# Kernel optimization log

Hardware: AMD Instinct MI355X
Metric: run time of the kernel (lower is better)

Reference implementation:

```python
import jax, jax.numpy as jnp
import numpy as np
import math

B, T, D, H = 4, 2048, 1024, 16
HD = D // H  # head_dim = 64

def setup_inputs() -> dict:
    key = jax.random.key(0)
    k1, k2, k3, k4, k5 = jax.random.split(key, 5)
    s = 1.0 / math.sqrt(D)
    return {
        "x": jax.random.normal(k1, (B, T, D), dtype=jnp.float32),
        "W_qkv": jax.random.normal(k2, (D, 3 * D), dtype=jnp.float32) * s,
        "b_qkv": jax.random.normal(k3, (3 * D,), dtype=jnp.float32) * 0.01,
        "W_fc": jax.random.normal(k4, (D, D), dtype=jnp.float32) * s,
        "b_fc": jax.random.normal(k5, (D,), dtype=jnp.float32) * 0.01,
    }

def reference(x, W_qkv, b_qkv, W_fc, b_fc):
    Bx, Tx, C = x.shape
    qkv = x @ W_qkv + b_qkv                                   # [B,T,3D]
    qkv = qkv.reshape(Bx, Tx, 3, H, HD)
    q, k, v = qkv[:, :, 0], qkv[:, :, 1], qkv[:, :, 2]        # [B,T,H,hd]
    scale = 1.0 / math.sqrt(HD)
    scores = jnp.einsum('bqhd,bkhd->bhqk', q, k) * scale      # [B,H,T,T]
    causal = jnp.tril(jnp.ones((Tx, Tx), dtype=bool))
    scores = jnp.where(causal, scores, -jnp.inf)
    weights = jax.nn.softmax(scores, axis=-1)
    out = jnp.einsum('bhqk,bkhd->bqhd', weights, v).reshape(Bx, Tx, C)
    return out @ W_fc + b_fc
```

## Files before the change

kernel.cpp:

```cpp
#include <hip/hip_runtime.h>
#include <hip/hip_bf16.h>

typedef __hip_bfloat16 bf16;
typedef short bf16x8 __attribute__((ext_vector_type(8)));
typedef float f32x4 __attribute__((ext_vector_type(4)));


static __device__ __forceinline__ void glds16(const bf16* g, bf16* l) {
  __builtin_amdgcn_global_load_lds(
      (const __attribute__((address_space(1))) void*)g,
      (__attribute__((address_space(3))) void*)l, 16, 0, 0);
}

static __device__ __forceinline__ unsigned short f2b(float f) {
  return __builtin_bit_cast(unsigned short, __float2bfloat16(f));
}
static __device__ __forceinline__ float b2f(unsigned int u16bits) {
  return __builtin_bit_cast(float, u16bits << 16);
}
static __device__ __forceinline__ float ex2(float x) {
  return __builtin_amdgcn_exp2f(x);
}

__global__ void k_convert(const float* __restrict__ in, unsigned short* __restrict__ out, int n4) {
  int i = blockIdx.x * 256 + threadIdx.x;
  if (i >= n4) return;
  float4 v = reinterpret_cast<const float4*>(in)[i];
  ushort4 o;
  o.x = f2b(v.x); o.y = f2b(v.y); o.z = f2b(v.z); o.w = f2b(v.w);
  reinterpret_cast<ushort4*>(out)[i] = o;
}

__global__ void k_transpose(const float* __restrict__ in, bf16* __restrict__ out, int R, int C) {
  __shared__ float t[32][33];
  int c0 = blockIdx.x * 32, r0 = blockIdx.y * 32;
  int tx = threadIdx.x, ty = threadIdx.y;
  #pragma unroll
  for (int j = 0; j < 32; j += 8)
    t[ty + j][tx] = in[(size_t)(r0 + ty + j) * C + c0 + tx];
  __syncthreads();
  #pragma unroll
  for (int j = 0; j < 32; j += 8)
    out[(size_t)(c0 + ty + j) * R + r0 + tx] = __float2bfloat16(t[tx][ty + j]);
}

template<int EPI>
__global__ __launch_bounds__(256, 2)
void k_gemm(const bf16* __restrict__ A, const bf16* __restrict__ Bt,
            const float* __restrict__ bias,
            bf16* __restrict__ Qh, bf16* __restrict__ Kh, bf16* __restrict__ Vt,
            float* __restrict__ Out)
{
  constexpr int K = 1024;
  __shared__ bf16 sA[128 * 32];
  __shared__ bf16 sB[128 * 32];
  const int tid = threadIdx.x;
  const int wv = tid >> 6, lane = tid & 63;
  const int wr = wv >> 1, wc = wv & 1;
  const int l4 = lane >> 4, l15 = lane & 15;

  const int nbx = gridDim.x;
  const int nwg = nbx * gridDim.y;
  const int flat = blockIdx.y * nbx + blockIdx.x;
  const int cpx = nwg >> 3;
  const int swz = (flat & 7) * cpx + (flat >> 3);
  const int bx = swz % nbx;
  const int by = swz / nbx;

  const int srow = lane >> 2;
  const int scol = (lane & 3) * 8;
  const bf16* gA0 = A  + (size_t)(by * 128 + wv * 16 + srow) * K + scol;
  const bf16* gB0 = Bt + (size_t)(bx * 128 + wv * 16 + srow) * K + scol;
  bf16* lA0 = sA + wv * 16 * 32;
  bf16* lB0 = sB + wv * 16 * 32;

  f32x4 acc[4][4];
  #pragma unroll
  for (int i = 0; i < 4; ++i)
    #pragma unroll
    for (int j = 0; j < 4; ++j) acc[i][j] = f32x4{0.f, 0.f, 0.f, 0.f};

  for (int kb = 0; kb < K; kb += 32) {
    glds16(gA0 + kb,                   lA0);
    glds16(gA0 + kb + (size_t)64 * K,  lA0 + 64 * 32);
    glds16(gB0 + kb,                   lB0);
    glds16(gB0 + kb + (size_t)64 * K,  lB0 + 64 * 32);
    __syncthreads();
    bf16x8 af[4], bfr[4];
    #pragma unroll
    for (int i = 0; i < 4; ++i)
      af[i] = *reinterpret_cast<const bf16x8*>(sA + (wr * 64 + i * 16 + l15) * 32 + l4 * 8);
    #pragma unroll
    for (int j = 0; j < 4; ++j)
      bfr[j] = *reinterpret_cast<const bf16x8*>(sB + (wc * 64 + j * 16 + l15) * 32 + l4 * 8);
    #pragma unroll
    for (int i = 0; i < 4; ++i)
      #pragma unroll
      for (int j = 0; j < 4; ++j)
        acc[i][j] = __builtin_amdgcn_mfma_f32_16x16x32_bf16(af[i], bfr[j], acc[i][j], 0, 0, 0);
    __syncthreads();
  }

  if (EPI == 0) {
    #pragma unroll
    for (int j = 0; j < 4; ++j) {
      const int n = bx * 128 + wc * 64 + j * 16 + l15;
      const float bj = bias[n];
      const int s = n >> 10;
      const int hh = (n >> 6) & 15;
      const int d = n & 63;
      #pragma unroll
      for (int i = 0; i < 4; ++i) {
        #pragma unroll
        for (int r = 0; r < 4; ++r) {
          const int m = by * 128 + wr * 64 + i * 16 + l4 * 4 + r;
          const int bb = m >> 11, t = m & 2047;
          const bf16 o = __float2bfloat16(acc[i][j][r] + bj);
          if (s == 0)      Qh[((size_t)((bb * 16 + hh) * 2048 + t)) * 64 + d] = o;
          else if (s == 1) Kh[((size_t)((bb * 16 + hh) * 2048 + t)) * 64 + d] = o;
          else             Vt[((size_t)((bb * 16 + hh) * 64 + d)) * 2048 + t] = o;
        }
      }
    }
  } else {
    #pragma unroll
    for (int j = 0; j < 4; ++j) {
      const int n = bx * 128 + wc * 64 + j * 16 + l15;
      const float bj = bias[n];
      #pragma unroll
      for (int i = 0; i < 4; ++i)
        #pragma unroll
        for (int r = 0; r < 4; ++r) {
          const int m = by * 128 + wr * 64 + i * 16 + l4 * 4 + r;
          Out[(size_t)m * 1024 + n] = acc[i][j][r] + bj;
        }
    }
  }
}

__global__ __launch_bounds__(256, 3)
void k_attn(const bf16* __restrict__ Qh, const bf16* __restrict__ Kh,
            const bf16* __restrict__ Vt, bf16* __restrict__ Ao)
{
  __shared__ unsigned int smem[4608];
  const int tid = threadIdx.x;
  const int wv = tid >> 6, lane = tid & 63;
  const int l4 = lane >> 4, l15 = lane & 15;

  const int bid = blockIdx.x;
  const int xcd = bid & 7;
  const int idx = bid >> 3;
  const int g   = idx & 31;
  const int grp = idx >> 5;
  const int bh  = grp * 8 + xcd;
  const int b = bh >> 4, h = bh & 15;

  const int role = (wv + bid) & 3;
  const int qi = (role < 2) ? g : (63 - g);
  const int parity = role & 1;
  const int qbase = qi * 32;

  const bf16* Qp = Qh + (size_t)bh * 2048 * 64;
  const bf16* Kp = Kh + (size_t)bh * 2048 * 64;
  const bf16* Vp = Vt + (size_t)bh * 64 * 2048;
  bf16* Pw = (bf16*)smem + wv * (32 * 40);

  bf16x8 qa[2][2];
  #pragma unroll
  for (int i = 0; i < 2; ++i)
    #pragma unroll
    for (int kh = 0; kh < 2; ++kh)
      qa[i][kh] = *reinterpret_cast<const bf16x8*>(
          Qp + (size_t)(qbase + i * 16 + l15) * 64 + kh * 32 + l4 * 8);

  f32x4 o[2][4];
  float mr[2], lr[2];
  #pragma unroll
  for (int i = 0; i < 2; ++i) {
    #pragma unroll
    for (int jd = 0; jd < 4; ++jd) o[i][jd] = f32x4{0.f, 0.f, 0.f, 0.f};
    mr[i] = -1e30f; lr[i] = 0.f;
  }

  const int ktmax = (qbase + 31) >> 5;

  const int kt0 = (parity <= ktmax) ? parity : ktmax;
  bf16x8 kbf[2][2];
  #pragma unroll
  for (int j = 0; j < 2; ++j)
    #pragma unroll
    for (int kh = 0; kh < 2; ++kh)
      kbf[j][kh] = *reinterpret_cast<const bf16x8*>(
          Kp + (size_t)(kt0 * 32 + j * 16 + l15) * 64 + kh * 32 + l4 * 8);

  for (int kt = parity; kt <= ktmax; kt += 2) {
    const bool full = (kt * 32 + 31) <= qbase;

    f32x4 s[2][2];
    #pragma unroll
    for (int i = 0; i < 2; ++i)
      #pragma unroll
      for (int j = 0; j < 2; ++j) s[i][j] = f32x4{0.f, 0.f, 0.f, 0.f};
    #pragma unroll
    for (int j = 0; j < 2; ++j)
      #pragma unroll
      for (int i = 0; i < 2; ++i) {
        s[i][j] = __builtin_amdgcn_mfma_f32_16x16x32_bf16(kbf[j][0], qa[i][0], s[i][j], 0, 0, 0);
        s[i][j] = __builtin_amdgcn_mfma_f32_16x16x32_bf16(kbf[j][1], qa[i][1], s[i][j], 0, 0, 0);
      }

    bf16x8 vbf[4];
    #pragma unroll
    for (int jd = 0; jd < 4; ++jd)
      vbf[jd] = *reinterpret_cast<const bf16x8*>(
          Vp + (size_t)(jd * 16 + l15) * 2048 + kt * 32 + l4 * 8);

    #pragma unroll
    for (int i = 0; i < 2; ++i) {
      const int q = qbase + i * 16 + l15;
      #pragma unroll
      for (int j = 0; j < 2; ++j)
        #pragma unroll
        for (int r = 0; r < 4; ++r) {
          float v = s[i][j][r] * 0.18033688f;
          if (!full) {
            const int kk = kt * 32 + j * 16 + l4 * 4 + r;
            if (kk > q) v = -1e30f;
          }
          s[i][j][r] = v;
        }
    }

    #pragma unroll
    for (int i = 0; i < 2; ++i) {
      float mx = s[i][0][0];
      #pragma unroll
      for (int j = 0; j < 2; ++j)
        #pragma unroll
        for (int r = 0; r < 4; ++r)
          if (j + r > 0) mx = fmaxf(mx, s[i][j][r]);
      mx = fmaxf(mx, __shfl_xor(mx, 16));
      mx = fmaxf(mx, __shfl_xor(mx, 32));
      if (__any(mx > mr[i] + 8.f)) {
        const float mn = fmaxf(mr[i], mx);
        const float al = ex2(mr[i] - mn);
        mr[i] = mn;
        lr[i] *= al;
        float albc[4];
        #pragma unroll
        for (int r = 0; r < 4; ++r) albc[r] = __shfl(al, l4 * 4 + r);
        #pragma unroll
        for (int jd = 0; jd < 4; ++jd)
          #pragma unroll
          for (int r = 0; r < 4; ++r) o[i][jd][r] *= albc[r];
      }
      float ps = 0.f;
      #pragma unroll
      for (int j = 0; j < 2; ++j) {
        const float p0 = ex2(s[i][j][0] - mr[i]);
        const float p1 = ex2(s[i][j][1] - mr[i]);
        const float p2 = ex2(s[i][j][2] - mr[i]);
        const float p3 = ex2(s[i][j][3] - mr[i]);
        ps += (p0 + p1) + (p2 + p3);
        const unsigned int u0 = (unsigned int)f2b(p0) | ((unsigned int)f2b(p1) << 16);
        const unsigned int u1 = (unsigned int)f2b(p2) | ((unsigned int)f2b(p3) << 16);
        *reinterpret_cast<uint2*>(Pw + (i * 16 + l15) * 40 + j * 16 + l4 * 4) =
            make_uint2(u0, u1);
      }
      ps += __shfl_xor(ps, 16);
      ps += __shfl_xor(ps, 32);
      lr[i] += ps;
    }

    const int ktn = (kt + 2 <= ktmax) ? (kt + 2) : ktmax;
    #pragma unroll
    for (int j = 0; j < 2; ++j)
      #pragma unroll
      for (int kh = 0; kh < 2; ++kh)
        kbf[j][kh] = *reinterpret_cast<const bf16x8*>(
            Kp + (size_t)(ktn * 32 + j * 16 + l15) * 64 + kh * 32 + l4 * 8);

    bf16x8 pa[2];
    #pragma unroll
    for (int i = 0; i < 2; ++i)
      pa[i] = *reinterpret_cast<const bf16x8*>(Pw + (i * 16 + l15) * 40 + l4 * 8);
    #pragma unroll
    for (int jd = 0; jd < 4; ++jd)
      #pragma unroll
      for (int i = 0; i < 2; ++i)
        o[i][jd] = __builtin_amdgcn_mfma_f32_16x16x32_bf16(pa[i], vbf[jd], o[i][jd], 0, 0, 0);
  }

  float mrv[2][4], lrv[2][4];
  #pragma unroll
  for (int i = 0; i < 2; ++i)
    #pragma unroll
    for (int r = 0; r < 4; ++r) {
      mrv[i][r] = __shfl(mr[i], l4 * 4 + r);
      lrv[i][r] = __shfl(lr[i], l4 * 4 + r);
    }

  __syncthreads();
  unsigned int* reg0 = smem;
  unsigned int* reg1 = smem + 64 * 33;
  if (parity == 1) {
    unsigned int* p = ((role == 1) ? reg0 : reg1) + lane * 33;
    #pragma unroll
    for (int i = 0; i < 2; ++i)
      #pragma unroll
      for (int r = 0; r < 4; ++r) {
        p[i * 4 + r]     = __builtin_bit_cast(unsigned int, mrv[i][r]);
        p[8 + i * 4 + r] = __builtin_bit_cast(unsigned int, lrv[i][r]);
      }
    #pragma unroll
    for (int i = 0; i < 2; ++i)
      #pragma unroll
      for (int jd = 0; jd < 4; ++jd)
        #pragma unroll
        for (int rp = 0; rp < 2; ++rp) {
          unsigned int lo = f2b(o[i][jd][2 * rp]);
          unsigned int hi = f2b(o[i][jd][2 * rp + 1]);
          p[16 + (i * 4 + jd) * 2 + rp] = lo | (hi << 16);
        }
  }
  __syncthreads();
  if (parity == 0) {
    const unsigned int* p = ((role == 0) ? reg0 : reg1) + lane * 33;
    #pragma unroll
    for (int i = 0; i < 2; ++i)
      #pragma unroll
      for (int r = 0; r < 4; ++r) {
        const float m1 = __builtin_bit_cast(float, p[i * 4 + r]);
        const float l1 = __builtin_bit_cast(float, p[8 + i * 4 + r]);
        const float mm = fmaxf(mrv[i][r], m1);
        const float a0 = ex2(mrv[i][r] - mm);
        const float a1 = ex2(m1 - mm);
        const float inv = 1.f / (lrv[i][r] * a0 + l1 * a1);
        const int q = qbase + i * 16 + l4 * 4 + r;
        #pragma unroll
        for (int jd = 0; jd < 4; ++jd) {
          const unsigned int u = p[16 + (i * 4 + jd) * 2 + (r >> 1)];
          const float o1 = b2f((r & 1) ? (u >> 16) : (u & 0xffffu));
          const float val = (o[i][jd][r] * a0 + o1 * a1) * inv;
          Ao[(size_t)(b * 2048 + q) * 1024 + h * 64 + jd * 16 + l15] = __float2bfloat16(val);
        }
      }
  }
}

extern "C" void kernel_launch(void* const* d_in, const int* in_sizes, int n_in,
                              void* d_out, int out_size, void* d_ws, size_t ws_size,
                              hipStream_t stream)
{
  const float* x     = (const float*)d_in[0];
  const float* W_qkv = (const float*)d_in[1];
  const float* b_qkv = (const float*)d_in[2];
  const float* W_fc  = (const float*)d_in[3];
  const float* b_fc  = (const float*)d_in[4];
  float* out = (float*)d_out;

  char* ws = (char*)d_ws;
  bf16* x_bf = (bf16*)ws;  ws += (size_t)8192 * 1024 * 2;
  bf16* Wqt  = (bf16*)ws;  ws += (size_t)3072 * 1024 * 2;
  bf16* Wft  = (bf16*)ws;  ws += (size_t)1024 * 1024 * 2;
  bf16* Qh   = (bf16*)ws;  ws += (size_t)4 * 16 * 2048 * 64 * 2;
  bf16* Kh   = (bf16*)ws;  ws += (size_t)4 * 16 * 2048 * 64 * 2;
  bf16* Vt   = (bf16*)ws;  ws += (size_t)4 * 16 * 64 * 2048 * 2;
  bf16* Ao   = (bf16*)ws;  ws += (size_t)8192 * 1024 * 2;

  k_convert<<<8192, 256, 0, stream>>>(x, (unsigned short*)x_bf, 8192 * 1024 / 4);
  k_transpose<<<dim3(3072 / 32, 1024 / 32), dim3(32, 8), 0, stream>>>(W_qkv, Wqt, 1024, 3072);
  k_transpose<<<dim3(1024 / 32, 1024 / 32), dim3(32, 8), 0, stream>>>(W_fc, Wft, 1024, 1024);
  k_gemm<0><<<dim3(24, 64), 256, 0, stream>>>(x_bf, Wqt, b_qkv, Qh, Kh, Vt, nullptr);
  k_attn<<<2048, 256, 0, stream>>>(Qh, Kh, Vt, Ao);
  k_gemm<1><<<dim3(8, 64), 256, 0, stream>>>(Ao, Wft, b_fc, nullptr, nullptr, nullptr, out);
}
```

Before: 272.9 us.

## Split causal attention KV range across four waves per query tile

Each attention block now processes a single 32-row query tile, with its four waves striding over key tiles by four instead of pairing two query tiles with two waves each. Partial softmax states from three waves are merged through shared memory by the fourth, and the grid doubles. This aims for finer scheduling granularity and shorter per-wave loops, at the cost of idle waves on short causal rows, a heavier merge step and larger LDS use.

```diff
diff --git a/kernel.cpp b/kernel.cpp
--- a/kernel.cpp
+++ b/kernel.cpp
@@ -142,7 +142,7 @@
 void k_attn(const bf16* __restrict__ Qh, const bf16* __restrict__ Kh,
             const bf16* __restrict__ Vt, bf16* __restrict__ Ao)
 {
-  __shared__ unsigned int smem[4608];
+  __shared__ unsigned int smem[6336];
   const int tid = threadIdx.x;
   const int wv = tid >> 6, lane = tid & 63;
   const int l4 = lane >> 4, l15 = lane & 15;
@@ -150,14 +150,12 @@
   const int bid = blockIdx.x;
   const int xcd = bid & 7;
   const int idx = bid >> 3;
-  const int g   = idx & 31;
-  const int grp = idx >> 5;
+  const int qi  = idx & 63;
+  const int grp = idx >> 6;
   const int bh  = grp * 8 + xcd;
   const int b = bh >> 4, h = bh & 15;
 
   const int role = (wv + bid) & 3;
-  const int qi = (role < 2) ? g : (63 - g);
-  const int parity = role & 1;
   const int qbase = qi * 32;
 
   const bf16* Qp = Qh + (size_t)bh * 2048 * 64;
@@ -182,9 +180,9 @@
     mr[i] = -1e30f; lr[i] = 0.f;
   }
 
-  const int ktmax = (qbase + 31) >> 5;
-
-  const int kt0 = (parity <= ktmax) ? parity : ktmax;
+  const int ktmax = qi;
+
+  const int kt0 = (role <= ktmax) ? role : ktmax;
   bf16x8 kbf[2][2];
   #pragma unroll
   for (int j = 0; j < 2; ++j)
@@ -193,7 +191,7 @@
       kbf[j][kh] = *reinterpret_cast<const bf16x8*>(
           Kp + (size_t)(kt0 * 32 + j * 16 + l15) * 64 + kh * 32 + l4 * 8);
 
-  for (int kt = parity; kt <= ktmax; kt += 2) {
+  for (int kt = role; kt <= ktmax; kt += 4) {
     const bool full = (kt * 32 + 31) <= qbase;
 
     f32x4 s[2][2];
@@ -272,7 +270,7 @@
       lr[i] += ps;
     }
 
-    const int ktn = (kt + 2 <= ktmax) ? (kt + 2) : ktmax;
+    const int ktn = (kt + 4 <= ktmax) ? (kt + 4) : ktmax;
     #pragma unroll
     for (int j = 0; j < 2; ++j)
       #pragma unroll
@@ -301,10 +299,8 @@
     }
 
   __syncthreads();
-  unsigned int* reg0 = smem;
-  unsigned int* reg1 = smem + 64 * 33;
-  if (parity == 1) {
-    unsigned int* p = ((role == 1) ? reg0 : reg1) + lane * 33;
+  if (role != 0) {
+    unsigned int* p = smem + (role - 1) * (64 * 33) + lane * 33;
     #pragma unroll
     for (int i = 0; i < 2; ++i)
       #pragma unroll
@@ -324,24 +320,35 @@
         }
   }
   __syncthreads();
-  if (parity == 0) {
-    const unsigned int* p = ((role == 0) ? reg0 : reg1) + lane * 33;
+  if (role == 0) {
+    const unsigned int* p0 = smem + 0 * (64 * 33) + lane * 33;
+    const unsigned int* p1 = smem + 1 * (64 * 33) + lane * 33;
+    const unsigned int* p2 = smem + 2 * (64 * 33) + lane * 33;
     #pragma unroll
     for (int i = 0; i < 2; ++i)
       #pragma unroll
       for (int r = 0; r < 4; ++r) {
-        const float m1 = __builtin_bit_cast(float, p[i * 4 + r]);
-        const float l1 = __builtin_bit_cast(float, p[8 + i * 4 + r]);
-        const float mm = fmaxf(mrv[i][r], m1);
+        const float m1 = __builtin_bit_cast(float, p0[i * 4 + r]);
+        const float m2 = __builtin_bit_cast(float, p1[i * 4 + r]);
+        const float m3 = __builtin_bit_cast(float, p2[i * 4 + r]);
+        const float l1 = __builtin_bit_cast(float, p0[8 + i * 4 + r]);
+        const float l2 = __builtin_bit_cast(float, p1[8 + i * 4 + r]);
+        const float l3 = __builtin_bit_cast(float, p2[8 + i * 4 + r]);
+        const float mm = fmaxf(fmaxf(mrv[i][r], m1), fmaxf(m2, m3));
         const float a0 = ex2(mrv[i][r] - mm);
         const float a1 = ex2(m1 - mm);
-        const float inv = 1.f / (lrv[i][r] * a0 + l1 * a1);
+        const float a2 = ex2(m2 - mm);
+        const float a3 = ex2(m3 - mm);
+        const float inv = 1.f / (lrv[i][r] * a0 + l1 * a1 + l2 * a2 + l3 * a3);
         const int q = qbase + i * 16 + l4 * 4 + r;
         #pragma unroll
         for (int jd = 0; jd < 4; ++jd) {
-          const unsigned int u = p[16 + (i * 4 + jd) * 2 + (r >> 1)];
-          const float o1 = b2f((r & 1) ? (u >> 16) : (u & 0xffffu));
-          const float val = (o[i][jd][r] * a0 + o1 * a1) * inv;
+          const int ui = 16 + (i * 4 + jd) * 2 + (r >> 1);
+          const bool hi = (r & 1);
+          const float o1 = b2f(hi ? (p0[ui] >> 16) : (p0[ui] & 0xffffu));
+          const float o2 = b2f(hi ? (p1[ui] >> 16) : (p1[ui] & 0xffffu));
+          const float o3 = b2f(hi ? (p2[ui] >> 16) : (p2[ui] & 0xffffu));
+          const float val = (o[i][jd][r] * a0 + o1 * a1 + o2 * a2 + o3 * a3) * inv;
           Ao[(size_t)(b * 2048 + q) * 1024 + h * 64 + jd * 16 + l15] = __float2bfloat16(val);
         }
       }
@@ -372,6 +379,6 @@
   k_transpose<<<dim3(3072 / 32, 1024 / 32), dim3(32, 8), 0, stream>>>(W_qkv, Wqt, 1024, 3072);
   k_transpose<<<dim3(1024 / 32, 1024 / 32), dim3(32, 8), 0, stream>>>(W_fc, Wft, 1024, 1024);
   k_gemm<0><<<dim3(24, 64), 256, 0, stream>>>(x_bf, Wqt, b_qkv, Qh, Kh, Vt, nullptr);
-  k_attn<<<2048, 256, 0, stream>>>(Qh, Kh, Vt, Ao);
+  k_attn<<<4096, 256, 0, stream>>>(Qh, Kh, Vt, Ao);
   k_gemm<1><<<dim3(8, 64), 256, 0, stream>>>(Ao, Wft, b_fc, nullptr, nullptr, nullptr, out);
 }
```

After: 289.8 us. +6.2%, slower.

## Double GEMM K-tile to 64 with XOR-swizzled LDS and fold softmax scale into Q

Applied to the files above, without the earlier changes.

The GEMM kernel now stages a K depth of 64 per iteration instead of 32, which halves the number of barrier pairs per output tile. The shared-memory layout gets an XOR swizzle on the 16-byte granules so fragment reads avoid bank conflicts. The softmax scale factor (1/sqrt(d) times log2 e) is folded into Q in the QKV epilogue, removing one multiply per score element in the attention inner loop. In exchange, LDS use per block doubles, and rounding Q to bf16 after scaling slightly changes numerics.

```diff
diff --git a/kernel.cpp b/kernel.cpp
--- a/kernel.cpp
+++ b/kernel.cpp
@@ -52,8 +52,8 @@
             float* __restrict__ Out)
 {
   constexpr int K = 1024;
-  __shared__ bf16 sA[128 * 32];
-  __shared__ bf16 sB[128 * 32];
+  __shared__ bf16 sA[128 * 64];
+  __shared__ bf16 sB[128 * 64];
   const int tid = threadIdx.x;
   const int wv = tid >> 6, lane = tid & 63;
   const int wr = wv >> 1, wc = wv & 1;
@@ -67,12 +67,12 @@
   const int bx = swz % nbx;
   const int by = swz / nbx;
 
-  const int srow = lane >> 2;
-  const int scol = (lane & 3) * 8;
-  const bf16* gA0 = A  + (size_t)(by * 128 + wv * 16 + srow) * K + scol;
-  const bf16* gB0 = Bt + (size_t)(bx * 128 + wv * 16 + srow) * K + scol;
-  bf16* lA0 = sA + wv * 16 * 32;
-  bf16* lB0 = sB + wv * 16 * 32;
+  const int srow8 = lane >> 3;
+  const int sgran = (lane & 7) ^ srow8;
+  const bf16* gA0 = A  + (size_t)(by * 128 + wv * 8 + srow8) * K + sgran * 8;
+  const bf16* gB0 = Bt + (size_t)(bx * 128 + wv * 8 + srow8) * K + sgran * 8;
+  bf16* lA0 = sA + wv * 8 * 64;
+  bf16* lB0 = sB + wv * 8 * 64;
 
   f32x4 acc[4][4];
   #pragma unroll
@@ -80,24 +80,34 @@
     #pragma unroll
     for (int j = 0; j < 4; ++j) acc[i][j] = f32x4{0.f, 0.f, 0.f, 0.f};
 
-  for (int kb = 0; kb < K; kb += 32) {
-    glds16(gA0 + kb,                   lA0);
-    glds16(gA0 + kb + (size_t)64 * K,  lA0 + 64 * 32);
-    glds16(gB0 + kb,                   lB0);
-    glds16(gB0 + kb + (size_t)64 * K,  lB0 + 64 * 32);
+  for (int kb = 0; kb < K; kb += 64) {
+    #pragma unroll
+    for (int c = 0; c < 4; ++c) {
+      glds16(gA0 + kb + (size_t)(c * 32) * K, lA0 + c * 32 * 64);
+      glds16(gB0 + kb + (size_t)(c * 32) * K, lB0 + c * 32 * 64);
+    }
     __syncthreads();
-    bf16x8 af[4], bfr[4];
-    #pragma unroll
-    for (int i = 0; i < 4; ++i)
-      af[i] = *reinterpret_cast<const bf16x8*>(sA + (wr * 64 + i * 16 + l15) * 32 + l4 * 8);
-    #pragma unroll
-    for (int j = 0; j < 4; ++j)
-      bfr[j] = *reinterpret_cast<const bf16x8*>(sB + (wc * 64 + j * 16 + l15) * 32 + l4 * 8);
-    #pragma unroll
-    for (int i = 0; i < 4; ++i)
-      #pragma unroll
-      for (int j = 0; j < 4; ++j)
-        acc[i][j] = __builtin_amdgcn_mfma_f32_16x16x32_bf16(af[i], bfr[j], acc[i][j], 0, 0, 0);
+    #pragma unroll
+    for (int kk = 0; kk < 2; ++kk) {
+      bf16x8 af[4], bfr[4];
+      #pragma unroll
+      for (int i = 0; i < 4; ++i) {
+        const int R = wr * 64 + i * 16 + l15;
+        af[i] = *reinterpret_cast<const bf16x8*>(
+            sA + R * 64 + (((kk * 4 + l4) ^ (R & 7)) * 8));
+      }
+      #pragma unroll
+      for (int j = 0; j < 4; ++j) {
+        const int R = wc * 64 + j * 16 + l15;
+        bfr[j] = *reinterpret_cast<const bf16x8*>(
+            sB + R * 64 + (((kk * 4 + l4) ^ (R & 7)) * 8));
+      }
+      #pragma unroll
+      for (int i = 0; i < 4; ++i)
+        #pragma unroll
+        for (int j = 0; j < 4; ++j)
+          acc[i][j] = __builtin_amdgcn_mfma_f32_16x16x32_bf16(af[i], bfr[j], acc[i][j], 0, 0, 0);
+    }
     __syncthreads();
   }
 
@@ -115,7 +125,9 @@
         for (int r = 0; r < 4; ++r) {
           const int m = by * 128 + wr * 64 + i * 16 + l4 * 4 + r;
           const int bb = m >> 11, t = m & 2047;
-          const bf16 o = __float2bfloat16(acc[i][j][r] + bj);
+          float of = acc[i][j][r] + bj;
+          if (s == 0) of *= 0.18033688f;
+          const bf16 o = __float2bfloat16(of);
           if (s == 0)      Qh[((size_t)((bb * 16 + hh) * 2048 + t)) * 64 + d] = o;
           else if (s == 1) Kh[((size_t)((bb * 16 + hh) * 2048 + t)) * 64 + d] = o;
           else             Vt[((size_t)((bb * 16 + hh) * 64 + d)) * 2048 + t] = o;
@@ -222,7 +234,7 @@
       for (int j = 0; j < 2; ++j)
         #pragma unroll
         for (int r = 0; r < 4; ++r) {
-          float v = s[i][j][r] * 0.18033688f;
+          float v = s[i][j][r];
           if (!full) {
             const int kk = kt * 32 + j * 16 + l4 * 4 + r;
             if (kk > q) v = -1e30f;
```

Result: faster. 265.8 us (-2.6%).
